# Performance work log

Measured on AMD Instinct MI355X. Metric: run time of the kernel, lower is better.

Reference implementation:

```python
import jax, jax.numpy as jnp
import numpy as np


def setup_inputs() -> dict:
    key = jax.random.key(0)
    k1, k2 = jax.random.split(key)
    q_embed = jax.random.normal(k1, (1000, 1024), dtype=jnp.float32)      # (V, D)
    conv_feat = jax.random.normal(k2, (64, 1024, 800), dtype=jnp.float32)  # (B, D, T)
    return {"q_embed": q_embed, "conv_feat": conv_feat}


def reference(q_embed, conv_feat):
    # sim_scores: (B, V, T) = q_embed (V, D) @ conv_feat (B, D, T), no scaling
    sim_scores = jnp.einsum('vd,bdt->bvt', q_embed, conv_feat)
    attention_weights = jax.nn.softmax(sim_scores, axis=2)  # over T
    # context: (B, V, D) = weights (B, V, T) @ conv_feat^T (B, T, D)
    context_vector = jnp.einsum('bvt,bdt->bvd', attention_weights, conv_feat)
    return (context_vector, attention_weights)
```

## Files before the change

kernel.cpp:

```cpp
#include <hip/hip_runtime.h>
#include <hip/hip_bf16.h>

typedef short bf16x8 __attribute__((ext_vector_type(8)));
typedef float f32x4 __attribute__((ext_vector_type(4)));

#define NV 1000
#define ND 1024
#define NT 800
#define NB 64

__device__ inline unsigned short f32_bf16(float f) {
    unsigned u = __builtin_bit_cast(unsigned, f);
    return (unsigned short)((u + 0x7FFFu + ((u >> 16) & 1u)) >> 16);
}
__device__ inline void split_bf16(float f, unsigned short& h, unsigned short& l) {
    unsigned u = __builtin_bit_cast(unsigned, f);
    unsigned hb = (u + 0x7FFFu + ((u >> 16) & 1u)) >> 16;
    h = (unsigned short)hb;
    float hf = __builtin_bit_cast(float, hb << 16);
    float lf = f - hf;
    unsigned ul = __builtin_bit_cast(unsigned, lf);
    l = (unsigned short)((ul + 0x7FFFu + ((ul >> 16) & 1u)) >> 16);
}

__device__ inline void gload16(const void* g, void* l) {
    __builtin_amdgcn_global_load_lds(
        (const __attribute__((address_space(1))) unsigned int*)g,
        (__attribute__((address_space(3))) unsigned int*)l, 16, 0, 0);
}

__global__ __launch_bounds__(256) void prep_q(const float* __restrict__ Q,
                                              unsigned short* __restrict__ Qh,
                                              unsigned short* __restrict__ Ql) {
    int idx = blockIdx.x * 256 + threadIdx.x;
    int row = idx >> 8;
    int c4 = (idx & 255) << 2;
    float4 f = make_float4(0.f, 0.f, 0.f, 0.f);
    if (row < NV) f = *(const float4*)(Q + (size_t)row * ND + c4);
    unsigned short h0,h1,h2,h3,l0,l1,l2,l3;
    split_bf16(f.x,h0,l0); split_bf16(f.y,h1,l1);
    split_bf16(f.z,h2,l2); split_bf16(f.w,h3,l3);
    *(ushort4*)(Qh + (size_t)row * ND + c4) = make_ushort4(h0,h1,h2,h3);
    *(ushort4*)(Ql + (size_t)row * ND + c4) = make_ushort4(l0,l1,l2,l3);
}

__global__ __launch_bounds__(256) void prep_c(const float* __restrict__ C,
                                              unsigned short* __restrict__ Cth,
                                              unsigned short* __restrict__ Ctl,
                                              unsigned short* __restrict__ Cbf,
                                              int writeCbf) {
    const int dt = blockIdx.x;
    const int tt = blockIdx.y;
    const int b  = blockIdx.z;
    const int tid = threadIdx.x;
    __shared__ float T[64][33];
    const float* Cb = C + (size_t)b * ND * NT;
    const int d0 = dt * 64, t0 = tt * 32;
#pragma unroll
    for (int r = 0; r < 2; ++r) {
        int idx = r * 256 + tid;
        int row = idx >> 3;
        int c4 = (idx & 7) << 2;
        float4 f = *(const float4*)(Cb + (size_t)(d0 + row) * NT + t0 + c4);
        T[row][c4 + 0] = f.x; T[row][c4 + 1] = f.y;
        T[row][c4 + 2] = f.z; T[row][c4 + 3] = f.w;
        if (writeCbf) {
            *(ushort4*)(Cbf + ((size_t)b * ND + d0 + row) * NT + t0 + c4) =
                make_ushort4(f32_bf16(f.x), f32_bf16(f.y), f32_bf16(f.z), f32_bf16(f.w));
        }
    }
    __syncthreads();
#pragma unroll
    for (int r = 0; r < 2; ++r) {
        int idx = r * 256 + tid;
        int trow = idx >> 4;
        int dc = (idx & 15) << 2;
        unsigned short h[4], l[4];
#pragma unroll
        for (int j = 0; j < 4; ++j) split_bf16(T[dc + j][trow], h[j], l[j]);
        size_t o = ((size_t)b * NT + t0 + trow) * ND + d0 + dc;
        *(ushort4*)(Cth + o) = make_ushort4(h[0],h[1],h[2],h[3]);
        *(ushort4*)(Ctl + o) = make_ushort4(l[0],l[1],l[2],l[3]);
    }
}

__global__ __launch_bounds__(256) void gemm1_kernel(const unsigned short* __restrict__ Qh,
                                                    const unsigned short* __restrict__ Ql,
                                                    const unsigned short* __restrict__ Cth,
                                                    const unsigned short* __restrict__ Ctl,
                                                    float* __restrict__ S) {
    const int h = blockIdx.x;
    const int L = (h & 7) * 320 + (h >> 3);
    const int bm = L & 7;
    const int rest = L >> 3;
    const int bn = rest % 5;
    const int b  = rest / 5;

    const int tid = threadIdx.x;
    const int lane = tid & 63;
    const int w = tid >> 6;
    const int wr = w >> 1, wc = w & 1;

    __shared__ unsigned short lds[2 * 18432];

    const int v0 = bm * 128, t0 = bn * 160;
    const unsigned short* Agh = Qh + (size_t)v0 * ND;
    const unsigned short* Agl = Ql + (size_t)v0 * ND;
    const unsigned short* Bgh = Cth + ((size_t)b * NT + t0) * ND;
    const unsigned short* Bgl = Ctl + ((size_t)b * NT + t0) * ND;

    f32x4 acc[4][5];
#pragma unroll
    for (int i = 0; i < 4; ++i)
#pragma unroll
        for (int j = 0; j < 5; ++j) acc[i][j] = (f32x4){0.f, 0.f, 0.f, 0.f};

    const int srow = lane >> 2;
    const int sslot = lane & 3;
    const int swz = (sslot ^ (srow & 3) ^ ((srow >> 2) & 3)) << 3;
    const int g = lane >> 4, rl = lane & 15;
    const int sx = (g ^ (rl & 3) ^ ((rl >> 2) & 3)) << 4;

    const unsigned short* srcB[9];
    int dstU[9];
#pragma unroll
    for (int j = 0; j < 9; ++j) {
        int R = w * 9 + j;
        const unsigned short* sp; int du;
        if (R < 8)       { sp = Agh + (size_t)(R * 16 + srow) * ND;          du = R * 512; }
        else if (R < 16) { sp = Agl + (size_t)((R - 8) * 16 + srow) * ND;    du = 4096 + (R - 8) * 512; }
        else if (R < 26) { sp = Bgh + (size_t)((R - 16) * 16 + srow) * ND;   du = 8192 + (R - 16) * 512; }
        else             { sp = Bgl + (size_t)((R - 26) * 16 + srow) * ND;   du = 13312 + (R - 26) * 512; }
        srcB[j] = sp + swz;
        dstU[j] = du;
    }

#define G1_STAGE(K0, BUF)                                                     \
    {                                                                         \
        unsigned short* Lb = lds + (BUF) * 18432;                             \
        _Pragma("unroll")                                                     \
        for (int j = 0; j < 9; ++j) gload16(srcB[j] + (K0), Lb + dstU[j]);    \
    }

#define G1_COMPUTE(BUF)                                                       \
    {                                                                         \
        const char* Lb = (const char*)(lds + (BUF) * 18432);                  \
        bf16x8 ah[4], al[4], bh[5], bl[5];                                    \
        _Pragma("unroll")                                                     \
        for (int mf = 0; mf < 4; ++mf) {                                      \
            int off = (wr * 64 + mf * 16 + rl) * 64 + sx;                     \
            ah[mf] = *(const bf16x8*)(Lb + off);                              \
            al[mf] = *(const bf16x8*)(Lb + 8192 + off);                       \
        }                                                                     \
        _Pragma("unroll")                                                     \
        for (int nf = 0; nf < 5; ++nf) {                                      \
            int off = (wc * 80 + nf * 16 + rl) * 64 + sx;                     \
            bh[nf] = *(const bf16x8*)(Lb + 16384 + off);                      \
            bl[nf] = *(const bf16x8*)(Lb + 26624 + off);                      \
        }                                                                     \
        _Pragma("unroll")                                                     \
        for (int mf = 0; mf < 4; ++mf)                                        \
            _Pragma("unroll")                                                 \
            for (int nf = 0; nf < 5; ++nf) {                                  \
                acc[mf][nf] = __builtin_amdgcn_mfma_f32_16x16x32_bf16(ah[mf], bh[nf], acc[mf][nf], 0, 0, 0); \
                acc[mf][nf] = __builtin_amdgcn_mfma_f32_16x16x32_bf16(ah[mf], bl[nf], acc[mf][nf], 0, 0, 0); \
                acc[mf][nf] = __builtin_amdgcn_mfma_f32_16x16x32_bf16(al[mf], bh[nf], acc[mf][nf], 0, 0, 0); \
            }                                                                 \
    }

    G1_STAGE(0, 0);
    int cur = 0;
#pragma unroll 1
    for (int t = 0; t < 31; ++t) {
        G1_STAGE((t + 1) * 32, cur ^ 1);
        asm volatile("s_waitcnt vmcnt(9)\n\ts_barrier" ::: "memory");
        G1_COMPUTE(cur);
        asm volatile("s_waitcnt lgkmcnt(0)\n\ts_barrier" ::: "memory");
        cur ^= 1;
    }
    asm volatile("s_waitcnt vmcnt(0)\n\ts_barrier" ::: "memory");
    G1_COMPUTE(cur);

    float* Sb = S + (size_t)b * NV * NT;
#pragma unroll
    for (int mf = 0; mf < 4; ++mf) {
#pragma unroll
        for (int nf = 0; nf < 5; ++nf) {
#pragma unroll
            for (int r = 0; r < 4; ++r) {
                int v = v0 + wr * 64 + mf * 16 + g * 4 + r;
                int t = t0 + wc * 80 + nf * 16 + rl;
                if (v < NV) Sb[(size_t)v * NT + t] = acc[mf][nf][r];
            }
        }
    }
#undef G1_STAGE
#undef G1_COMPUTE
}

__global__ __launch_bounds__(256) void softmax_kernel(float* __restrict__ S,
                                                      unsigned short* __restrict__ Wbf,
                                                      int writeWbf) {
    const int row = blockIdx.x * 4 + (threadIdx.x >> 6);
    const int lane = threadIdx.x & 63;
    float4* p4 = (float4*)(S + (size_t)row * NT);
    unsigned short* pw = Wbf + (size_t)row * NT;
    float4 v[4];
    float m = -INFINITY;
#pragma unroll
    for (int i = 0; i < 4; ++i) {
        int idx = i * 64 + lane;
        if (idx < 200) {
            v[i] = p4[idx];
            m = fmaxf(m, fmaxf(fmaxf(v[i].x, v[i].y), fmaxf(v[i].z, v[i].w)));
        }
    }
#pragma unroll
    for (int off = 32; off; off >>= 1) m = fmaxf(m, __shfl_xor(m, off));
    float s = 0.f;
#pragma unroll
    for (int i = 0; i < 4; ++i) {
        int idx = i * 64 + lane;
        if (idx < 200) {
            v[i].x = __expf(v[i].x - m); v[i].y = __expf(v[i].y - m);
            v[i].z = __expf(v[i].z - m); v[i].w = __expf(v[i].w - m);
            s += (v[i].x + v[i].y) + (v[i].z + v[i].w);
        }
    }
#pragma unroll
    for (int off = 32; off; off >>= 1) s += __shfl_xor(s, off);
    const float inv = 1.0f / s;
#pragma unroll
    for (int i = 0; i < 4; ++i) {
        int idx = i * 64 + lane;
        if (idx < 200) {
            float4 o = make_float4(v[i].x * inv, v[i].y * inv, v[i].z * inv, v[i].w * inv);
            p4[idx] = o;
            if (writeWbf)
                *(ushort4*)(pw + idx * 4) =
                    make_ushort4(f32_bf16(o.x), f32_bf16(o.y), f32_bf16(o.z), f32_bf16(o.w));
        }
    }
}

__global__ __launch_bounds__(512) void gemm2_fast(const unsigned short* __restrict__ Wbf,
                                                  const unsigned short* __restrict__ Cbf,
                                                  float* __restrict__ O) {
    const int h = blockIdx.x;
    const int L = (h & 7) * 128 + (h >> 3);
    const int b  = L >> 4;
    const int bm = (L >> 2) & 3;
    const int bn = L & 3;
    const int tid = threadIdx.x;
    const int lane = tid & 63;
    const int w = tid >> 6;
    const int wr = w >> 2, wc = w & 3;

    __shared__ unsigned short lds[2 * 16384];

    const int v0 = bm * 256, d0 = bn * 256;
    const unsigned short* Ag = Wbf + (size_t)b * NV * NT;
    const unsigned short* Bg = Cbf + ((size_t)b * ND + d0) * NT;

    f32x4 acc[8][4];
#pragma unroll
    for (int i = 0; i < 8; ++i)
#pragma unroll
        for (int j = 0; j < 4; ++j) acc[i][j] = (f32x4){0.f, 0.f, 0.f, 0.f};

    const int srow = lane >> 2;
    const int sslot = lane & 3;
    const int swz = (sslot ^ (srow & 3) ^ ((srow >> 2) & 3)) << 3;
    const int g = lane >> 4, rl = lane & 15;
    const int sx = (g ^ (rl & 3) ^ ((rl >> 2) & 3)) << 4;

#define G2_STAGE(K0, BUF)                                                     \
    {                                                                         \
        unsigned short* Lb = lds + (BUF) * 16384;                             \
        _Pragma("unroll")                                                     \
        for (int i = w; i < 16; i += 8) {                                     \
            int row = i * 16 + srow;                                          \
            int vrow = v0 + row; if (vrow > NV - 1) vrow = NV - 1;            \
            gload16(Ag + (size_t)vrow * NT + swz + (K0), Lb + i * 512);       \
            gload16(Bg + (size_t)row * NT + swz + (K0), Lb + 8192 + i * 512); \
        }                                                                     \
    }

#define G2_COMPUTE(BUF)                                                       \
    {                                                                         \
        const char* Lb = (const char*)(lds + (BUF) * 16384);                  \
        bf16x8 a[8], bq[4];                                                   \
        _Pragma("unroll")                                                     \
        for (int mf = 0; mf < 8; ++mf) {                                      \
            int off = (wr * 128 + mf * 16 + rl) * 64 + sx;                    \
            a[mf] = *(const bf16x8*)(Lb + off);                               \
        }                                                                     \
        _Pragma("unroll")                                                     \
        for (int nf = 0; nf < 4; ++nf) {                                      \
            int off = (wc * 64 + nf * 16 + rl) * 64 + sx;                     \
            bq[nf] = *(const bf16x8*)(Lb + 16384 + off);                      \
        }                                                                     \
        _Pragma("unroll")                                                     \
        for (int mf = 0; mf < 8; ++mf)                                        \
            _Pragma("unroll")                                                 \
            for (int nf = 0; nf < 4; ++nf)                                    \
                acc[mf][nf] = __builtin_amdgcn_mfma_f32_16x16x32_bf16(a[mf], bq[nf], acc[mf][nf], 0, 0, 0); \
    }

    G2_STAGE(0, 0);
    int cur = 0;
#pragma unroll 1
    for (int t = 0; t < 24; ++t) {
        G2_STAGE((t + 1) * 32, cur ^ 1);
        asm volatile("s_waitcnt vmcnt(4)\n\ts_barrier" ::: "memory");
        G2_COMPUTE(cur);
        asm volatile("s_waitcnt lgkmcnt(0)\n\ts_barrier" ::: "memory");
        cur ^= 1;
    }
    asm volatile("s_waitcnt vmcnt(0)\n\ts_barrier" ::: "memory");
    G2_COMPUTE(cur);

    float* Ob = O + (size_t)b * NV * ND;
#pragma unroll
    for (int mf = 0; mf < 8; ++mf) {
#pragma unroll
        for (int nf = 0; nf < 4; ++nf) {
#pragma unroll
            for (int r = 0; r < 4; ++r) {
                int v = v0 + wr * 128 + mf * 16 + g * 4 + r;
                int d = d0 + wc * 64 + nf * 16 + rl;
                if (v < NV) Ob[(size_t)v * ND + d] = acc[mf][nf][r];
            }
        }
    }
#undef G2_STAGE
#undef G2_COMPUTE
}

__global__ __launch_bounds__(256) void gemm2_mid(const unsigned short* __restrict__ Wbf,
                                                 const float* __restrict__ C,
                                                 float* __restrict__ O) {
    const int h = blockIdx.x;
    const int L = (h & 7) * 512 + (h >> 3);
    const int bm = L & 7;
    const int bn = (L >> 3) & 7;
    const int b  = L >> 6;
    const int tid = threadIdx.x;
    const int lane = tid & 63;
    const int w = tid >> 6;
    const int wr = w >> 1, wc = w & 1;

    __shared__ unsigned short As[128 * 32];
    __shared__ unsigned short Bs[128][40];

    const int v0 = bm * 128, d0 = bn * 128;
    const unsigned short* Ag = Wbf + (size_t)b * NV * NT;
    const float* Cb = C + (size_t)b * ND * NT;

    f32x4 acc[4][4];
#pragma unroll
    for (int i = 0; i < 4; ++i)
#pragma unroll
        for (int j = 0; j < 4; ++j) acc[i][j] = (f32x4){0.f, 0.f, 0.f, 0.f};

    const int srow = lane >> 2;
    const int sslot = lane & 3;

    for (int k0 = 0; k0 < NT; k0 += 32) {
        for (int i = w; i < 8; i += 4) {
            int row = i * 16 + srow;
            int c = ((sslot ^ (row & 3)) << 3) + k0;
            int vrow = v0 + row; if (vrow > NV - 1) vrow = NV - 1;
            gload16(Ag + (size_t)vrow * NT + c, As + i * 512);
        }
#pragma unroll
        for (int r = 0; r < 4; ++r) {
            int idx = r * 256 + tid;
            int row = idx >> 3;
            int kq  = (idx & 7) << 2;
            const float4 f = *(const float4*)(Cb + (size_t)(d0 + row) * NT + k0 + kq);
            *(ushort4*)&Bs[row][kq] = make_ushort4(f32_bf16(f.x), f32_bf16(f.y), f32_bf16(f.z), f32_bf16(f.w));
        }
        __syncthreads();

        const int g = lane >> 4, rl = lane & 15;
        const int sx = (g ^ (rl & 3)) << 4;
        const int kk = g << 3;
        bf16x8 a[4], bfr[4];
#pragma unroll
        for (int mf = 0; mf < 4; ++mf) {
            int off = (wr * 64 + mf * 16 + rl) * 64 + sx;
            a[mf] = *(const bf16x8*)((const char*)As + off);
        }
#pragma unroll
        for (int nf = 0; nf < 4; ++nf) {
            int row = wc * 64 + nf * 16 + rl;
            bfr[nf] = *(const bf16x8*)&Bs[row][kk];
        }
#pragma unroll
        for (int mf = 0; mf < 4; ++mf)
#pragma unroll
            for (int nf = 0; nf < 4; ++nf)
                acc[mf][nf] = __builtin_amdgcn_mfma_f32_16x16x32_bf16(a[mf], bfr[nf], acc[mf][nf], 0, 0, 0);
        __syncthreads();
    }

    float* Ob = O + (size_t)b * NV * ND;
    const int g = lane >> 4, rl = lane & 15;
#pragma unroll
    for (int mf = 0; mf < 4; ++mf) {
#pragma unroll
        for (int nf = 0; nf < 4; ++nf) {
#pragma unroll
            for (int r = 0; r < 4; ++r) {
                int v = v0 + wr * 64 + mf * 16 + g * 4 + r;
                int d = d0 + wc * 64 + nf * 16 + rl;
                if (v < NV) Ob[(size_t)v * ND + d] = acc[mf][nf][r];
            }
        }
    }
}

__global__ __launch_bounds__(256) void gemm2_slow(const float* __restrict__ W,
                                                  const float* __restrict__ C,
                                                  float* __restrict__ O) {
    const int h = blockIdx.x;
    const int L = (h & 7) * 512 + (h >> 3);
    const int bm = L & 7;
    const int bn = (L >> 3) & 7;
    const int b  = L >> 6;
    const int tid = threadIdx.x;
    const int lane = tid & 63;
    const int wid = tid >> 6;
    const int wr = wid >> 1;
    const int wc = wid & 1;

    __shared__ unsigned short As[128][40];
    __shared__ unsigned short Bs[128][40];

    const float* Wb = W + (size_t)b * NV * NT;
    const float* Cb = C + (size_t)b * ND * NT;
    const int v0 = bm * 128;
    const int d0 = bn * 128;

    f32x4 acc[4][4];
#pragma unroll
    for (int i = 0; i < 4; ++i)
#pragma unroll
        for (int j = 0; j < 4; ++j) acc[i][j] = (f32x4){0.f, 0.f, 0.f, 0.f};

    for (int k0 = 0; k0 < NT; k0 += 32) {
#pragma unroll
        for (int r = 0; r < 4; ++r) {
            int idx = r * 256 + tid;
            int row = idx >> 3;
            int kq  = (idx & 7) << 2;
            int v = v0 + row; if (v > NV - 1) v = NV - 1;
            const float4 f = *(const float4*)(Wb + (size_t)v * NT + k0 + kq);
            *(ushort4*)&As[row][kq] = make_ushort4(f32_bf16(f.x), f32_bf16(f.y), f32_bf16(f.z), f32_bf16(f.w));
        }
#pragma unroll
        for (int r = 0; r < 4; ++r) {
            int idx = r * 256 + tid;
            int row = idx >> 3;
            int kq  = (idx & 7) << 2;
            const float4 f = *(const float4*)(Cb + (size_t)(d0 + row) * NT + k0 + kq);
            *(ushort4*)&Bs[row][kq] = make_ushort4(f32_bf16(f.x), f32_bf16(f.y), f32_bf16(f.z), f32_bf16(f.w));
        }
        __syncthreads();

        bf16x8 a[4], bfr[4];
        const int kk = (lane >> 4) << 3;
#pragma unroll
        for (int mf = 0; mf < 4; ++mf) {
            int row = wr * 64 + mf * 16 + (lane & 15);
            a[mf] = *(const bf16x8*)&As[row][kk];
        }
#pragma unroll
        for (int nf = 0; nf < 4; ++nf) {
            int row = wc * 64 + nf * 16 + (lane & 15);
            bfr[nf] = *(const bf16x8*)&Bs[row][kk];
        }
#pragma unroll
        for (int mf = 0; mf < 4; ++mf)
#pragma unroll
            for (int nf = 0; nf < 4; ++nf)
                acc[mf][nf] = __builtin_amdgcn_mfma_f32_16x16x32_bf16(a[mf], bfr[nf], acc[mf][nf], 0, 0, 0);
        __syncthreads();
    }

    float* Ob = O + (size_t)b * NV * ND;
#pragma unroll
    for (int mf = 0; mf < 4; ++mf) {
#pragma unroll
        for (int nf = 0; nf < 4; ++nf) {
#pragma unroll
            for (int r = 0; r < 4; ++r) {
                int v = v0 + wr * 64 + mf * 16 + (lane >> 4) * 4 + r;
                int d = d0 + wc * 64 + nf * 16 + (lane & 15);
                if (v < NV) Ob[(size_t)v * ND + d] = acc[mf][nf][r];
            }
        }
    }
}

extern "C" void kernel_launch(void* const* d_in, const int* in_sizes, int n_in,
                              void* d_out, int out_size, void* d_ws, size_t ws_size,
                              hipStream_t stream) {
    const float* Q = (const float*)d_in[0];
    const float* C = (const float*)d_in[1];
    float* ctx = (float*)d_out;
    float* wts = ctx + (size_t)NB * NV * ND;

    unsigned short* Cth = (unsigned short*)ctx;
    unsigned short* Ctl = Cth + (size_t)NB * NT * ND;
    unsigned short* Qh  = Ctl + (size_t)NB * NT * ND;
    unsigned short* Ql  = Qh + (size_t)1024 * ND;

    const size_t WbfBytes = (size_t)NB * NV * NT * 2;
    const size_t CbfBytes = (size_t)NB * ND * NT * 2;
    unsigned short* Wbf = (unsigned short*)d_ws;
    unsigned short* Cbf = (unsigned short*)((char*)d_ws + WbfBytes);
    const int wsFast = ws_size >= WbfBytes + CbfBytes;
    const int wsMid  = ws_size >= WbfBytes;

    prep_q<<<dim3(1024), 256, 0, stream>>>(Q, Qh, Ql);
    prep_c<<<dim3(16, 25, NB), 256, 0, stream>>>(C, Cth, Ctl, Cbf, wsFast);
    gemm1_kernel<<<dim3(2560), 256, 0, stream>>>(Qh, Ql, Cth, Ctl, wts);
    softmax_kernel<<<dim3(16000), 256, 0, stream>>>(wts, Wbf, wsMid);
    if (wsFast)      gemm2_fast<<<dim3(1024), 512, 0, stream>>>(Wbf, Cbf, ctx);
    else if (wsMid)  gemm2_mid<<<dim3(4096), 256, 0, stream>>>(Wbf, C, ctx);
    else             gemm2_slow<<<dim3(4096), 256, 0, stream>>>(wts, C, ctx);
}
```

Measured before the change: 685.5 us.

## Simplify gemm1 to single-buffered loop; deepen gemm2 pipeline to four stages

gemm1 drops its hand-written double-buffered async pipeline and returns to a simple load, __syncthreads, compute, __syncthreads loop with separate LDS arrays. gemm2 moves from two to four LDS buffers with three stages in flight, interleaves its A-fragment loads with MFMA groups, and raises wave priority around the MFMAs. The gemm2 change is meant to hide more global-load latency. The gemm1 change removes load/compute overlap and will likely slow that kernel, and the larger LDS footprint in gemm2 may reduce occupancy.

```diff
diff --git a/kernel.cpp b/kernel.cpp
--- a/kernel.cpp
+++ b/kernel.cpp
@@ -101,7 +101,10 @@
     const int w = tid >> 6;
     const int wr = w >> 1, wc = w & 1;
 
-    __shared__ unsigned short lds[2 * 18432];
+    __shared__ unsigned short Ah[128 * 32];
+    __shared__ unsigned short Al[128 * 32];
+    __shared__ unsigned short Bh[160 * 32];
+    __shared__ unsigned short Bl[160 * 32];
 
     const int v0 = bm * 128, t0 = bn * 160;
     const unsigned short* Agh = Qh + (size_t)v0 * ND;
@@ -118,70 +121,48 @@
     const int srow = lane >> 2;
     const int sslot = lane & 3;
     const int swz = (sslot ^ (srow & 3) ^ ((srow >> 2) & 3)) << 3;
+
+    for (int k0 = 0; k0 < ND; k0 += 32) {
+        for (int i = w; i < 8; i += 4) {
+            int row = i * 16 + srow;
+            gload16(Agh + (size_t)row * ND + swz + k0, Ah + i * 512);
+            gload16(Agl + (size_t)row * ND + swz + k0, Al + i * 512);
+        }
+        for (int i = w; i < 10; i += 4) {
+            int row = i * 16 + srow;
+            gload16(Bgh + (size_t)row * ND + swz + k0, Bh + i * 512);
+            gload16(Bgl + (size_t)row * ND + swz + k0, Bl + i * 512);
+        }
+        __syncthreads();
+
+        const int g = lane >> 4, rl = lane & 15;
+        const int sx = (g ^ (rl & 3) ^ ((rl >> 2) & 3)) << 4;
+        bf16x8 ah[4], al[4], bh[5], bl[5];
+#pragma unroll
+        for (int mf = 0; mf < 4; ++mf) {
+            int off = (wr * 64 + mf * 16 + rl) * 64 + sx;
+            ah[mf] = *(const bf16x8*)((const char*)Ah + off);
+            al[mf] = *(const bf16x8*)((const char*)Al + off);
+        }
+#pragma unroll
+        for (int nf = 0; nf < 5; ++nf) {
+            int off = (wc * 80 + nf * 16 + rl) * 64 + sx;
+            bh[nf] = *(const bf16x8*)((const char*)Bh + off);
+            bl[nf] = *(const bf16x8*)((const char*)Bl + off);
+        }
+#pragma unroll
+        for (int mf = 0; mf < 4; ++mf)
+#pragma unroll
+            for (int nf = 0; nf < 5; ++nf) {
+                acc[mf][nf] = __builtin_amdgcn_mfma_f32_16x16x32_bf16(ah[mf], bh[nf], acc[mf][nf], 0, 0, 0);
+                acc[mf][nf] = __builtin_amdgcn_mfma_f32_16x16x32_bf16(ah[mf], bl[nf], acc[mf][nf], 0, 0, 0);
+                acc[mf][nf] = __builtin_amdgcn_mfma_f32_16x16x32_bf16(al[mf], bh[nf], acc[mf][nf], 0, 0, 0);
+            }
+        __syncthreads();
+    }
+
+    float* Sb = S + (size_t)b * NV * NT;
     const int g = lane >> 4, rl = lane & 15;
-    const int sx = (g ^ (rl & 3) ^ ((rl >> 2) & 3)) << 4;
-
-    const unsigned short* srcB[9];
-    int dstU[9];
-#pragma unroll
-    for (int j = 0; j < 9; ++j) {
-        int R = w * 9 + j;
-        const unsigned short* sp; int du;
-        if (R < 8)       { sp = Agh + (size_t)(R * 16 + srow) * ND;          du = R * 512; }
-        else if (R < 16) { sp = Agl + (size_t)((R - 8) * 16 + srow) * ND;    du = 4096 + (R - 8) * 512; }
-        else if (R < 26) { sp = Bgh + (size_t)((R - 16) * 16 + srow) * ND;   du = 8192 + (R - 16) * 512; }
-        else             { sp = Bgl + (size_t)((R - 26) * 16 + srow) * ND;   du = 13312 + (R - 26) * 512; }
-        srcB[j] = sp + swz;
-        dstU[j] = du;
-    }
-
-#define G1_STAGE(K0, BUF)                                                     \
-    {                                                                         \
-        unsigned short* Lb = lds + (BUF) * 18432;                             \
-        _Pragma("unroll")                                                     \
-        for (int j = 0; j < 9; ++j) gload16(srcB[j] + (K0), Lb + dstU[j]);    \
-    }
-
-#define G1_COMPUTE(BUF)                                                       \
-    {                                                                         \
-        const char* Lb = (const char*)(lds + (BUF) * 18432);                  \
-        bf16x8 ah[4], al[4], bh[5], bl[5];                                    \
-        _Pragma("unroll")                                                     \
-        for (int mf = 0; mf < 4; ++mf) {                                      \
-            int off = (wr * 64 + mf * 16 + rl) * 64 + sx;                     \
-            ah[mf] = *(const bf16x8*)(Lb + off);                              \
-            al[mf] = *(const bf16x8*)(Lb + 8192 + off);                       \
-        }                                                                     \
-        _Pragma("unroll")                                                     \
-        for (int nf = 0; nf < 5; ++nf) {                                      \
-            int off = (wc * 80 + nf * 16 + rl) * 64 + sx;                     \
-            bh[nf] = *(const bf16x8*)(Lb + 16384 + off);                      \
-            bl[nf] = *(const bf16x8*)(Lb + 26624 + off);                      \
-        }                                                                     \
-        _Pragma("unroll")                                                     \
-        for (int mf = 0; mf < 4; ++mf)                                        \
-            _Pragma("unroll")                                                 \
-            for (int nf = 0; nf < 5; ++nf) {                                  \
-                acc[mf][nf] = __builtin_amdgcn_mfma_f32_16x16x32_bf16(ah[mf], bh[nf], acc[mf][nf], 0, 0, 0); \
-                acc[mf][nf] = __builtin_amdgcn_mfma_f32_16x16x32_bf16(ah[mf], bl[nf], acc[mf][nf], 0, 0, 0); \
-                acc[mf][nf] = __builtin_amdgcn_mfma_f32_16x16x32_bf16(al[mf], bh[nf], acc[mf][nf], 0, 0, 0); \
-            }                                                                 \
-    }
-
-    G1_STAGE(0, 0);
-    int cur = 0;
-#pragma unroll 1
-    for (int t = 0; t < 31; ++t) {
-        G1_STAGE((t + 1) * 32, cur ^ 1);
-        asm volatile("s_waitcnt vmcnt(9)\n\ts_barrier" ::: "memory");
-        G1_COMPUTE(cur);
-        asm volatile("s_waitcnt lgkmcnt(0)\n\ts_barrier" ::: "memory");
-        cur ^= 1;
-    }
-    asm volatile("s_waitcnt vmcnt(0)\n\ts_barrier" ::: "memory");
-    G1_COMPUTE(cur);
-
-    float* Sb = S + (size_t)b * NV * NT;
 #pragma unroll
     for (int mf = 0; mf < 4; ++mf) {
 #pragma unroll
@@ -194,8 +175,6 @@
             }
         }
     }
-#undef G1_STAGE
-#undef G1_COMPUTE
 }
 
 __global__ __launch_bounds__(256) void softmax_kernel(float* __restrict__ S,
@@ -256,7 +235,7 @@
     const int w = tid >> 6;
     const int wr = w >> 2, wc = w & 3;
 
-    __shared__ unsigned short lds[2 * 16384];
+    __shared__ unsigned short lds[4 * 16384];
 
     const int v0 = bm * 256, d0 = bn * 256;
     const unsigned short* Ag = Wbf + (size_t)b * NV * NT;
@@ -289,36 +268,43 @@
 #define G2_COMPUTE(BUF)                                                       \
     {                                                                         \
         const char* Lb = (const char*)(lds + (BUF) * 16384);                  \
-        bf16x8 a[8], bq[4];                                                   \
+        bf16x8 bq[4];                                                         \
         _Pragma("unroll")                                                     \
-        for (int mf = 0; mf < 8; ++mf) {                                      \
-            int off = (wr * 128 + mf * 16 + rl) * 64 + sx;                    \
-            a[mf] = *(const bf16x8*)(Lb + off);                               \
-        }                                                                     \
+        for (int nf = 0; nf < 4; ++nf)                                        \
+            bq[nf] = *(const bf16x8*)(Lb + 16384 + (wc * 64 + nf * 16 + rl) * 64 + sx); \
         _Pragma("unroll")                                                     \
-        for (int nf = 0; nf < 4; ++nf) {                                      \
-            int off = (wc * 64 + nf * 16 + rl) * 64 + sx;                     \
-            bq[nf] = *(const bf16x8*)(Lb + 16384 + off);                      \
-        }                                                                     \
-        _Pragma("unroll")                                                     \
-        for (int mf = 0; mf < 8; ++mf)                                        \
+        for (int p = 0; p < 4; ++p) {                                         \
+            bf16x8 a0 = *(const bf16x8*)(Lb + (wr * 128 + (2 * p) * 16 + rl) * 64 + sx);     \
+            bf16x8 a1 = *(const bf16x8*)(Lb + (wr * 128 + (2 * p + 1) * 16 + rl) * 64 + sx); \
+            __builtin_amdgcn_s_setprio(1);                                    \
             _Pragma("unroll")                                                 \
             for (int nf = 0; nf < 4; ++nf)                                    \
-                acc[mf][nf] = __builtin_amdgcn_mfma_f32_16x16x32_bf16(a[mf], bq[nf], acc[mf][nf], 0, 0, 0); \
+                acc[2 * p][nf] = __builtin_amdgcn_mfma_f32_16x16x32_bf16(a0, bq[nf], acc[2 * p][nf], 0, 0, 0); \
+            _Pragma("unroll")                                                 \
+            for (int nf = 0; nf < 4; ++nf)                                    \
+                acc[2 * p + 1][nf] = __builtin_amdgcn_mfma_f32_16x16x32_bf16(a1, bq[nf], acc[2 * p + 1][nf], 0, 0, 0); \
+            __builtin_amdgcn_s_setprio(0);                                    \
+        }                                                                     \
     }
 
     G2_STAGE(0, 0);
-    int cur = 0;
+    G2_STAGE(32, 1);
+    G2_STAGE(64, 2);
 #pragma unroll 1
-    for (int t = 0; t < 24; ++t) {
-        G2_STAGE((t + 1) * 32, cur ^ 1);
-        asm volatile("s_waitcnt vmcnt(4)\n\ts_barrier" ::: "memory");
-        G2_COMPUTE(cur);
+    for (int t = 0; t < 22; ++t) {
+        G2_STAGE((t + 3) * 32, (t + 3) & 3);
+        asm volatile("s_waitcnt vmcnt(12)\n\ts_barrier" ::: "memory");
+        G2_COMPUTE(t & 3);
         asm volatile("s_waitcnt lgkmcnt(0)\n\ts_barrier" ::: "memory");
-        cur ^= 1;
-    }
+    }
+    asm volatile("s_waitcnt vmcnt(8)\n\ts_barrier" ::: "memory");
+    G2_COMPUTE(22 & 3);
+    asm volatile("s_waitcnt lgkmcnt(0)\n\ts_barrier" ::: "memory");
+    asm volatile("s_waitcnt vmcnt(4)\n\ts_barrier" ::: "memory");
+    G2_COMPUTE(23 & 3);
+    asm volatile("s_waitcnt lgkmcnt(0)\n\ts_barrier" ::: "memory");
     asm volatile("s_waitcnt vmcnt(0)\n\ts_barrier" ::: "memory");
-    G2_COMPUTE(cur);
+    G2_COMPUTE(24 & 3);
 
     float* Ob = O + (size_t)b * NV * ND;
 #pragma unroll
```

Measured after the change: 671.0 us. -2.1%, faster.
